# Kernel optimization log

Measured on AMD Instinct MI355X. Metric: run time of the kernel, lower is better.

The kernel has to match this reference:

```python
import jax, jax.numpy as jnp
import numpy as np

NUM_HEADS = 32
HIDDEN = 4096
HEAD_DIM = HIDDEN // NUM_HEADS
BATCH = 1
SEQ = 2048


def setup_inputs() -> dict:
    key = jax.random.key(0)
    ks = jax.random.split(key, 8)
    hidden_states = jax.random.normal(ks[0], (BATCH, SEQ, HIDDEN), dtype=jnp.float32)
    residual = jax.random.normal(ks[1], (BATCH, SEQ, HIDDEN), dtype=jnp.float32)
    # BLOOM alibi: [batch*heads, 1, kv_len], broadcast over q_length in baddbmm
    alibi = jax.random.normal(ks[2], (BATCH * NUM_HEADS, 1, SEQ), dtype=jnp.float32) * 0.1
    # causal boolean mask: True = masked (filled with -inf before softmax)
    attention_mask = ~jnp.tril(jnp.ones((SEQ, SEQ), dtype=bool))[None, None, :, :]
    scale = 0.02
    Wqkv = jax.random.normal(ks[3], (3 * HIDDEN, HIDDEN), dtype=jnp.float32) * scale
    bqkv = jax.random.normal(ks[4], (3 * HIDDEN,), dtype=jnp.float32) * scale
    Wd = jax.random.normal(ks[5], (HIDDEN, HIDDEN), dtype=jnp.float32) * scale
    bd = jax.random.normal(ks[6], (HIDDEN,), dtype=jnp.float32) * scale
    return {"hidden_states": hidden_states, "residual": residual, "alibi": alibi,
            "attention_mask": attention_mask, "Wqkv": Wqkv, "bqkv": bqkv,
            "Wd": Wd, "bd": bd}


def reference(hidden_states, residual, alibi, attention_mask, Wqkv, bqkv, Wd, bd):
    B, S, H = hidden_states.shape
    nh, hd = NUM_HEADS, HEAD_DIM
    inv_norm = 1.0 / np.sqrt(hd).astype(np.float32)

    # fused QKV projection, BLOOM interleaved layout [B, S, nh, 3, hd]
    fused = hidden_states @ Wqkv.T + bqkv           # [B, S, 3H]
    fused = fused.reshape(B, S, nh, 3, hd)
    q = jnp.transpose(fused[..., 0, :], (0, 2, 1, 3))  # [B, nh, S, hd]
    k = jnp.transpose(fused[..., 1, :], (0, 2, 1, 3))  # [B, nh, S, hd]
    v = jnp.transpose(fused[..., 2, :], (0, 2, 1, 3))  # [B, nh, S, hd]

    # baddbmm: alibi + inv_norm * Q @ K^T
    alibi_b = alibi.reshape(B, nh, 1, S)                # broadcast over q_length
    scores = alibi_b + inv_norm * jnp.einsum('bhqd,bhkd->bhqk', q, k)
    scores = jnp.where(attention_mask, jnp.finfo(scores.dtype).min, scores)
    probs = jax.nn.softmax(scores, axis=-1)             # [B, nh, S, S]

    ctx = jnp.einsum('bhqk,bhkd->bhqd', probs, v)       # [B, nh, S, hd]
    ctx = jnp.transpose(ctx, (0, 2, 1, 3)).reshape(B, S, H)
    out = ctx @ Wd.T + bd
    return residual + out
```

## Files before the change

kernel.cpp:

```cpp
#include <hip/hip_runtime.h>


#define SEQL 2048
#define HIDN 4096
#define NHEAD 32
#define HDIM 128
#define H3 12288

typedef __bf16 bf16x8 __attribute__((ext_vector_type(8)));
typedef float f32x4 __attribute__((ext_vector_type(4)));
typedef unsigned short u16x8 __attribute__((ext_vector_type(8)));

__device__ __forceinline__ unsigned short f2bf(float f) {
  union { float f; unsigned u; } v; v.f = f;
  return (unsigned short)((v.u + 0x7FFFu + ((v.u >> 16) & 1u)) >> 16);
}

__device__ __forceinline__ void gload_lds16(const void* g, void* l) {
  __builtin_amdgcn_global_load_lds(
      (const __attribute__((address_space(1))) void*)g,
      (__attribute__((address_space(3))) void*)l, 16, 0, 0);
}

__global__ __launch_bounds__(256) void cvt_f32_bf16(
    const float* __restrict__ in, unsigned short* __restrict__ out, long long n) {
  long long i = ((long long)blockIdx.x * blockDim.x + threadIdx.x) * 8;
  long long stride = (long long)gridDim.x * blockDim.x * 8;
  for (; i < n; i += stride) {
    float4 a = *(const float4*)(in + i);
    float4 b = *(const float4*)(in + i + 4);
    u16x8 o;
    o[0] = f2bf(a.x); o[1] = f2bf(a.y); o[2] = f2bf(a.z); o[3] = f2bf(a.w);
    o[4] = f2bf(b.x); o[5] = f2bf(b.y); o[6] = f2bf(b.z); o[7] = f2bf(b.w);
    *(u16x8*)(out + i) = o;
  }
}

template <int EPI>
__global__ __launch_bounds__(256) void gemm_nt(
    const unsigned short* __restrict__ A, const unsigned short* __restrict__ B,
    int M, int N, int K,
    const float* __restrict__ bias, const float* __restrict__ residual,
    float* __restrict__ outf,
    unsigned short* __restrict__ q_bf, unsigned short* __restrict__ k_bf,
    unsigned short* __restrict__ v_t) {
  __shared__ unsigned short As[128 * 64];
  __shared__ unsigned short Bs[128 * 64];

  const int tid = threadIdx.x;
  const int l = tid & 63;
  const int w = tid >> 6;
  const int wr = (w >> 1) * 64;
  const int wc = (w & 1) * 64;
  const int tm0 = blockIdx.x * 128;
  const int tn0 = blockIdx.y * 128;

  const int lr = l >> 3;
  const int lc = (l & 7) ^ lr;

  f32x4 acc[4][4] = {};

  for (int kt = 0; kt < K; kt += 64) {
    __syncthreads();
#pragma unroll
    for (int i = 0; i < 4; ++i) {
      const int row = w * 32 + i * 8 + lr;
      gload_lds16(&A[(long long)(tm0 + row) * K + kt + lc * 8],
                  (char*)As + (w * 4 + i) * 1024);
      gload_lds16(&B[(long long)(tn0 + row) * K + kt + lc * 8],
                  (char*)Bs + (w * 4 + i) * 1024);
    }
    __syncthreads();
#pragma unroll
    for (int kk = 0; kk < 2; ++kk) {
      const int colb = kk * 64 + (l >> 4) * 16;
      bf16x8 af[4], bfr[4];
#pragma unroll
      for (int m = 0; m < 4; ++m) {
        int row = wr + m * 16 + (l & 15);
        af[m] = *(const bf16x8*)((char*)As + row * 128 + (colb ^ ((row & 7) << 4)));
      }
#pragma unroll
      for (int n = 0; n < 4; ++n) {
        int row = wc + n * 16 + (l & 15);
        bfr[n] = *(const bf16x8*)((char*)Bs + row * 128 + (colb ^ ((row & 7) << 4)));
      }
#pragma unroll
      for (int m = 0; m < 4; ++m)
#pragma unroll
        for (int n = 0; n < 4; ++n)
          acc[m][n] = __builtin_amdgcn_mfma_f32_16x16x32_bf16(af[m], bfr[n], acc[m][n], 0, 0, 0);
    }
  }

#pragma unroll
  for (int m = 0; m < 4; ++m) {
#pragma unroll
    for (int n = 0; n < 4; ++n) {
      const int col = tn0 + wc + n * 16 + (l & 15);
      const float bv = bias[col];
#pragma unroll
      for (int r = 0; r < 4; ++r) {
        const int rowg = tm0 + wr + m * 16 + (l >> 4) * 4 + r;
        float v = acc[m][n][r] + bv;
        if (EPI == 0) {
          const int head = col / 384;
          const int rem = col - head * 384;
          const int which = rem >> 7;
          const int d = rem & 127;
          const unsigned short bv16 = f2bf(v);
          if (which == 0)
            q_bf[(long long)(head * SEQL + rowg) * HDIM + d] = bv16;
          else if (which == 1)
            k_bf[(long long)(head * SEQL + rowg) * HDIM + d] = bv16;
          else
            v_t[(long long)(head * HDIM + d) * SEQL + rowg] = bv16;
        } else {
          const long long idx = (long long)rowg * N + col;
          outf[idx] = v + residual[idx];
        }
      }
    }
  }
}

__global__ __launch_bounds__(256) void attn_fwd(
    const unsigned short* __restrict__ q_bf, const unsigned short* __restrict__ k_bf,
    const unsigned short* __restrict__ v_t, const float* __restrict__ alibi,
    unsigned short* __restrict__ ctx_bf) {
  __shared__ unsigned short Ks[64 * 128];
  __shared__ unsigned short Vs[128 * 64];
  __shared__ unsigned short Ps[4][16 * 64];
  __shared__ float Al[SEQL];

  const int tid = threadIdx.x;
  const int l = tid & 63;
  const int w = tid >> 6;
  const int h = blockIdx.x;
  const int qt = blockIdx.y * 64;
  const int qw = qt + w * 16;

  for (int i = tid; i < SEQL; i += 256) Al[i] = alibi[h * SEQL + i];

  bf16x8 qf[4];
  {
    const unsigned short* qp =
        &q_bf[(long long)(h * SEQL + qw + (l & 15)) * HDIM + (l >> 4) * 8];
#pragma unroll
    for (int kk = 0; kk < 4; ++kk) qf[kk] = *(const bf16x8*)(qp + kk * 32);
  }

  f32x4 oacc[8] = {};
  float mrun[4] = {-__builtin_inff(), -__builtin_inff(), -__builtin_inff(), -__builtin_inff()};
  float lrun[4] = {0.f, 0.f, 0.f, 0.f};
  const float inv_norm = 0.08838834764831845f;

  const int kR = l >> 4, kC = l & 15;
  const int vR = l >> 3, vC = (l & 7) ^ vR;

  const int ntiles = blockIdx.y + 1;
  for (int t = 0; t < ntiles; ++t) {
    const int kv0 = t * 64;
    __syncthreads();
#pragma unroll
    for (int i = 0; i < 4; ++i) {
      const int krow = w * 16 + i * 4 + kR;
      const int ksrc = kC ^ ((i & 1) * 4 + kR);
      gload_lds16(&k_bf[(long long)(h * SEQL + kv0 + krow) * HDIM + ksrc * 8],
                  (char*)Ks + (w * 4 + i) * 1024);
      const int vrow = w * 32 + i * 8 + vR;
      gload_lds16(&v_t[(long long)(h * HDIM + vrow) * SEQL + kv0 + vC * 8],
                  (char*)Vs + (w * 4 + i) * 1024);
    }
    __syncthreads();

    f32x4 sacc[4] = {};
#pragma unroll
    for (int kk = 0; kk < 4; ++kk) {
      const int colb = kk * 64 + (l >> 4) * 16;
#pragma unroll
      for (int n = 0; n < 4; ++n) {
        int row = n * 16 + (l & 15);
        bf16x8 kf = *(const bf16x8*)((char*)Ks + row * 256 + (colb ^ ((row & 7) << 4)));
        sacc[n] = __builtin_amdgcn_mfma_f32_16x16x32_bf16(qf[kk], kf, sacc[n], 0, 0, 0);
      }
    }

    float sc[4][4];
#pragma unroll
    for (int n = 0; n < 4; ++n) {
      const int kv = kv0 + n * 16 + (l & 15);
      const float al = Al[kv];
#pragma unroll
      for (int r = 0; r < 4; ++r) {
        const int qrow = qw + (l >> 4) * 4 + r;
        float v = al + inv_norm * sacc[n][r];
        sc[n][r] = (kv > qrow) ? -__builtin_inff() : v;
      }
    }

#pragma unroll
    for (int r = 0; r < 4; ++r) {
      float m0 = fmaxf(fmaxf(sc[0][r], sc[1][r]), fmaxf(sc[2][r], sc[3][r]));
      m0 = fmaxf(m0, __shfl_xor(m0, 1, 64));
      m0 = fmaxf(m0, __shfl_xor(m0, 2, 64));
      m0 = fmaxf(m0, __shfl_xor(m0, 4, 64));
      m0 = fmaxf(m0, __shfl_xor(m0, 8, 64));
      const float mnew = fmaxf(mrun[r], m0);
      float p0 = 0.f;
#pragma unroll
      for (int n = 0; n < 4; ++n) {
        const float pv = __expf(sc[n][r] - mnew);
        sc[n][r] = pv;
        p0 += pv;
      }
      p0 += __shfl_xor(p0, 1, 64);
      p0 += __shfl_xor(p0, 2, 64);
      p0 += __shfl_xor(p0, 4, 64);
      p0 += __shfl_xor(p0, 8, 64);
      const float scale = __expf(mrun[r] - mnew);
      mrun[r] = mnew;
      lrun[r] = lrun[r] * scale + p0;
#pragma unroll
      for (int n2 = 0; n2 < 8; ++n2) oacc[n2][r] *= scale;
    }

#pragma unroll
    for (int n = 0; n < 4; ++n)
#pragma unroll
      for (int r = 0; r < 4; ++r) {
        const int row = (l >> 4) * 4 + r;
        const int colp = n * 16 + (l & 15);
        *(unsigned short*)((char*)Ps[w] + row * 128 + ((colp * 2) ^ ((row & 7) << 4))) =
            f2bf(sc[n][r]);
      }
    __threadfence_block();
    bf16x8 pf[2];
#pragma unroll
    for (int kk2 = 0; kk2 < 2; ++kk2) {
      const int row = l & 15;
      const int colb = kk2 * 64 + (l >> 4) * 16;
      pf[kk2] = *(const bf16x8*)((char*)Ps[w] + row * 128 + (colb ^ ((row & 7) << 4)));
    }

#pragma unroll
    for (int n2 = 0; n2 < 8; ++n2) {
#pragma unroll
      for (int kk2 = 0; kk2 < 2; ++kk2) {
        const int row = n2 * 16 + (l & 15);
        const int colb = kk2 * 64 + (l >> 4) * 16;
        bf16x8 vf = *(const bf16x8*)((char*)Vs + row * 128 + (colb ^ ((row & 7) << 4)));
        oacc[n2] = __builtin_amdgcn_mfma_f32_16x16x32_bf16(pf[kk2], vf, oacc[n2], 0, 0, 0);
      }
    }
  }

#pragma unroll
  for (int n2 = 0; n2 < 8; ++n2)
#pragma unroll
    for (int r = 0; r < 4; ++r) {
      const int qrow = qw + (l >> 4) * 4 + r;
      const int col = h * HDIM + n2 * 16 + (l & 15);
      ctx_bf[(long long)qrow * HIDN + col] = f2bf(oacc[n2][r] / lrun[r]);
    }
}

extern "C" void kernel_launch(void* const* d_in, const int* in_sizes, int n_in,
                              void* d_out, int out_size, void* d_ws, size_t ws_size,
                              hipStream_t stream) {
  const float* hidden = (const float*)d_in[0];
  const float* residual = (const float*)d_in[1];
  const float* alibi = (const float*)d_in[2];
  const float* Wqkv = (const float*)d_in[4];
  const float* bqkv = (const float*)d_in[5];
  const float* Wd = (const float*)d_in[6];
  const float* bd = (const float*)d_in[7];
  float* out = (float*)d_out;

  char* ws = (char*)d_ws;
  const size_t MB16 = 16777216;
  unsigned short* q_bf = (unsigned short*)(ws);
  unsigned short* k_bf = (unsigned short*)(ws + MB16);
  unsigned short* v_t = (unsigned short*)(ws + 2 * MB16);
  unsigned short* hid_bf = (unsigned short*)(ws + 3 * MB16);
  unsigned short* wqkv_bf = (unsigned short*)(ws + 4 * MB16);
  unsigned short* wd_bf = (unsigned short*)(ws + 4 * MB16);
  unsigned short* ctx_bf = (unsigned short*)(ws + 4 * MB16 + 33554432);

  cvt_f32_bf16<<<4096, 256, 0, stream>>>(hidden, hid_bf, (long long)SEQL * HIDN);
  cvt_f32_bf16<<<24576, 256, 0, stream>>>(Wqkv, wqkv_bf, (long long)H3 * HIDN);

  gemm_nt<0><<<dim3(SEQL / 128, H3 / 128), 256, 0, stream>>>(
      hid_bf, wqkv_bf, SEQL, H3, HIDN, bqkv, nullptr, nullptr, q_bf, k_bf, v_t);

  cvt_f32_bf16<<<8192, 256, 0, stream>>>(Wd, wd_bf, (long long)HIDN * HIDN);

  attn_fwd<<<dim3(NHEAD, SEQL / 64), 256, 0, stream>>>(q_bf, k_bf, v_t, alibi, ctx_bf);

  gemm_nt<1><<<dim3(SEQL / 128, HIDN / 128), 256, 0, stream>>>(
      ctx_bf, wd_bf, SEQL, HIDN, HIDN, bd, residual, out, nullptr, nullptr, nullptr);
}
```

Measured before the change: 522.6 us.

## Replace QKV GEMM with 256x256-tile double-buffered 8-wave pipelined kernel

Adds a dedicated QKV projection kernel that uses 256x256 output tiles, 512 threads and double-buffered LDS staging. Global-to-LDS prefetches for the next K-step are interleaved with MFMA phases, ordered by explicit vmcnt waits and barriers, with setprio raised around the math. Block indices are swizzled for cache locality. The aim is more data reuse per tile and memory latency hidden behind compute in the largest GEMM. In exchange it uses more LDS and registers, and the hand-placed wait counts are fragile to get right. The output projection keeps the old kernel, now split into its own non-templated version.

```diff
diff --git a/kernel.cpp b/kernel.cpp
--- a/kernel.cpp
+++ b/kernel.cpp
@@ -36,14 +36,139 @@
   }
 }
 
-template <int EPI>
-__global__ __launch_bounds__(256) void gemm_nt(
+__global__ __launch_bounds__(512, 2) void gemm256_qkv(
+    const unsigned short* __restrict__ A, const unsigned short* __restrict__ B,
+    const float* __restrict__ bias,
+    unsigned short* __restrict__ q_bf, unsigned short* __restrict__ k_bf,
+    unsigned short* __restrict__ v_t) {
+  __shared__ unsigned short lds[2][2][2][8192];
+
+  const int tid = threadIdx.x;
+  const int l = tid & 63;
+  const int w = tid >> 6;
+  const int K = HIDN;
+
+  const int b = blockIdx.x;
+  const int lin = (b & 7) * 48 + (b >> 3);
+  const int tm0 = (lin & 7) * 256;
+  const int tn0 = (lin >> 3) * 256;
+
+  const int lr = l >> 3;
+  const int lc = (l & 7) ^ lr;
+  const int wm = (w >> 2) * 64;
+  const int wn = (w & 3) * 32;
+
+  f32x4 acc[2][2][4][2] = {};
+
+  auto stageA = [&](int bf, int mh, int kt) {
+#pragma unroll
+    for (int i = 0; i < 2; ++i) {
+      const int c = w * 2 + i;
+      gload_lds16(&A[(long long)(tm0 + mh * 128 + c * 8 + lr) * K + kt + lc * 8],
+                  (char*)&lds[bf][0][mh][0] + c * 1024);
+    }
+  };
+  auto stageB = [&](int bf, int nh, int kt) {
+#pragma unroll
+    for (int i = 0; i < 2; ++i) {
+      const int c = w * 2 + i;
+      gload_lds16(&B[(long long)(tn0 + nh * 128 + c * 8 + lr) * K + kt + lc * 8],
+                  (char*)&lds[bf][1][nh][0] + c * 1024);
+    }
+  };
+
+  stageA(0, 0, 0);
+  stageB(0, 0, 0);
+  stageB(0, 1, 0);
+  stageA(0, 1, 0);
+  asm volatile("s_waitcnt vmcnt(4)" ::: "memory");
+  __builtin_amdgcn_s_barrier();
+
+  const int NT = K / 64;
+  for (int t = 0; t < NT; ++t) {
+    const int bf = t & 1, nb = bf ^ 1;
+    const int kt1 = (t + 1) * 64;
+    const bool pf = (t + 1 < NT);
+#pragma unroll
+    for (int ph = 0; ph < 4; ++ph) {
+      const int mh = ph >> 1, nh = ph & 1;
+      bf16x8 af[4][2], bfr[2][2];
+#pragma unroll
+      for (int mi = 0; mi < 4; ++mi) {
+        const int r = wm + mi * 16 + (l & 15);
+#pragma unroll
+        for (int kk = 0; kk < 2; ++kk)
+          af[mi][kk] = *(const bf16x8*)((const char*)&lds[bf][0][mh][0] +
+              r * 128 + ((kk * 64 + (l >> 4) * 16) ^ ((l & 7) << 4)));
+      }
+#pragma unroll
+      for (int ni = 0; ni < 2; ++ni) {
+        const int r = wn + ni * 16 + (l & 15);
+#pragma unroll
+        for (int kk = 0; kk < 2; ++kk)
+          bfr[ni][kk] = *(const bf16x8*)((const char*)&lds[bf][1][nh][0] +
+              r * 128 + ((kk * 64 + (l >> 4) * 16) ^ ((l & 7) << 4)));
+      }
+      if (ph == 0) {
+        if (pf) { stageA(nb, 0, kt1); asm volatile("s_waitcnt vmcnt(4)" ::: "memory"); }
+        else    { asm volatile("s_waitcnt vmcnt(2)" ::: "memory"); }
+      } else if (ph == 1) {
+        if (pf) { stageB(nb, 0, kt1); asm volatile("s_waitcnt vmcnt(4)" ::: "memory"); }
+        else    { asm volatile("s_waitcnt vmcnt(0)" ::: "memory"); }
+      } else if (ph == 2) {
+        if (pf) { stageB(nb, 1, kt1); }
+      } else {
+        if (pf) { stageA(nb, 1, kt1); asm volatile("s_waitcnt vmcnt(4)" ::: "memory"); }
+      }
+      __builtin_amdgcn_s_barrier();
+      asm volatile("s_waitcnt lgkmcnt(0)" ::: "memory");
+      __builtin_amdgcn_s_setprio(1);
+#pragma unroll
+      for (int kk = 0; kk < 2; ++kk)
+#pragma unroll
+        for (int mi = 0; mi < 4; ++mi)
+#pragma unroll
+          for (int ni = 0; ni < 2; ++ni)
+            acc[mh][nh][mi][ni] = __builtin_amdgcn_mfma_f32_16x16x32_bf16(
+                af[mi][kk], bfr[ni][kk], acc[mh][nh][mi][ni], 0, 0, 0);
+      __builtin_amdgcn_s_setprio(0);
+      __builtin_amdgcn_s_barrier();
+    }
+  }
+
+#pragma unroll
+  for (int mh = 0; mh < 2; ++mh)
+#pragma unroll
+    for (int nh = 0; nh < 2; ++nh)
+#pragma unroll
+      for (int mi = 0; mi < 4; ++mi)
+#pragma unroll
+        for (int ni = 0; ni < 2; ++ni) {
+          const int col = tn0 + nh * 128 + wn + ni * 16 + (l & 15);
+          const float bv = bias[col];
+          const int head = col / 384;
+          const int rem = col - head * 384;
+          const int which = rem >> 7;
+          const int d = rem & 127;
+#pragma unroll
+          for (int r = 0; r < 4; ++r) {
+            const int row = tm0 + mh * 128 + wm + mi * 16 + (l >> 4) * 4 + r;
+            const unsigned short bv16 = f2bf(acc[mh][nh][mi][ni][r] + bv);
+            if (which == 0)
+              q_bf[(long long)(head * SEQL + row) * HDIM + d] = bv16;
+            else if (which == 1)
+              k_bf[(long long)(head * SEQL + row) * HDIM + d] = bv16;
+            else
+              v_t[(long long)(head * HDIM + d) * SEQL + row] = bv16;
+          }
+        }
+}
+
+__global__ __launch_bounds__(256) void gemm_nt_res(
     const unsigned short* __restrict__ A, const unsigned short* __restrict__ B,
     int M, int N, int K,
     const float* __restrict__ bias, const float* __restrict__ residual,
-    float* __restrict__ outf,
-    unsigned short* __restrict__ q_bf, unsigned short* __restrict__ k_bf,
-    unsigned short* __restrict__ v_t) {
+    float* __restrict__ outf) {
   __shared__ unsigned short As[128 * 64];
   __shared__ unsigned short Bs[128 * 64];
 
@@ -94,7 +219,7 @@
   }
 
 #pragma unroll
-  for (int m = 0; m < 4; ++m) {
+  for (int m = 0; m < 4; ++m)
 #pragma unroll
     for (int n = 0; n < 4; ++n) {
       const int col = tn0 + wc + n * 16 + (l & 15);
@@ -102,26 +227,10 @@
 #pragma unroll
       for (int r = 0; r < 4; ++r) {
         const int rowg = tm0 + wr + m * 16 + (l >> 4) * 4 + r;
-        float v = acc[m][n][r] + bv;
-        if (EPI == 0) {
-          const int head = col / 384;
-          const int rem = col - head * 384;
-          const int which = rem >> 7;
-          const int d = rem & 127;
-          const unsigned short bv16 = f2bf(v);
-          if (which == 0)
-            q_bf[(long long)(head * SEQL + rowg) * HDIM + d] = bv16;
-          else if (which == 1)
-            k_bf[(long long)(head * SEQL + rowg) * HDIM + d] = bv16;
-          else
-            v_t[(long long)(head * HDIM + d) * SEQL + rowg] = bv16;
-        } else {
-          const long long idx = (long long)rowg * N + col;
-          outf[idx] = v + residual[idx];
-        }
-      }
-    }
-  }
+        const long long idx = (long long)rowg * N + col;
+        outf[idx] = acc[m][n][r] + bv + residual[idx];
+      }
+    }
 }
 
 __global__ __launch_bounds__(256) void attn_fwd(
@@ -290,13 +399,12 @@
   cvt_f32_bf16<<<4096, 256, 0, stream>>>(hidden, hid_bf, (long long)SEQL * HIDN);
   cvt_f32_bf16<<<24576, 256, 0, stream>>>(Wqkv, wqkv_bf, (long long)H3 * HIDN);
 
-  gemm_nt<0><<<dim3(SEQL / 128, H3 / 128), 256, 0, stream>>>(
-      hid_bf, wqkv_bf, SEQL, H3, HIDN, bqkv, nullptr, nullptr, q_bf, k_bf, v_t);
+  gemm256_qkv<<<384, 512, 0, stream>>>(hid_bf, wqkv_bf, bqkv, q_bf, k_bf, v_t);
 
   cvt_f32_bf16<<<8192, 256, 0, stream>>>(Wd, wd_bf, (long long)HIDN * HIDN);
 
   attn_fwd<<<dim3(NHEAD, SEQL / 64), 256, 0, stream>>>(q_bf, k_bf, v_t, alibi, ctx_bf);
 
-  gemm_nt<1><<<dim3(SEQL / 128, HIDN / 128), 256, 0, stream>>>(
-      ctx_bf, wd_bf, SEQL, HIDN, HIDN, bd, residual, out, nullptr, nullptr, nullptr);
-}
+  gemm_nt_res<<<dim3(SEQL / 128, HIDN / 128), 256, 0, stream>>>(
+      ctx_bf, wd_bf, SEQL, HIDN, HIDN, bd, residual, out);
+}
```

Result: slower. 541.0 us (+3.5%).
